# Kernel tuning notes

Hardware: AMD Instinct MI355X
Metric: run time of the kernel (lower is better)

The kernel has to match this reference:

```python
import jax, jax.numpy as jnp
import numpy as np

EPS = 1e-5
NUM_GROUPS = 8


def setup_inputs() -> dict:
    key = jax.random.key(0)
    ks = jax.random.split(key, 7)
    B, C, D, H, W = 2, 128, 16, 16, 16
    s = 1.0 / np.sqrt(C)
    return {
        "x": jax.random.normal(ks[0], (B, C, D, H, W), dtype=jnp.float32),
        "Wq": jax.random.normal(ks[1], (C, C), dtype=jnp.float32) * s,
        "Wk": jax.random.normal(ks[2], (C, C), dtype=jnp.float32) * s,
        "Wv": jax.random.normal(ks[3], (C, C), dtype=jnp.float32) * s,
        "Wo": jax.random.normal(ks[4], (C, C), dtype=jnp.float32) * s,
        "gamma": jnp.ones((C,), dtype=jnp.float32),
        "beta": jnp.zeros((C,), dtype=jnp.float32),
    }


def reference(x, Wq, Wk, Wv, Wo, gamma, beta):
    B, C = x.shape[0], x.shape[1]
    spatial = x.shape[2:]
    xf = x.reshape(B, C, -1)  # [B, C, N]

    # 1x1 conv == channel-mixing matmul
    q = jnp.einsum('oc,bcn->bon', Wq, xf)
    k = jnp.einsum('oc,bcn->bon', Wk, xf)
    v = jnp.einsum('oc,bcn->bon', Wv, xf)

    # unscaled attention: qk[b,n,m] = sum_c q[b,c,n] k[b,c,m]
    w = jax.nn.softmax(jnp.einsum('bcn,bcm->bnm', q, k), axis=-1)  # [B, N, N]
    # h = v @ w^T : h[b,c,n] = sum_m v[b,c,m] w[b,n,m]
    h = jnp.einsum('bcm,bnm->bcn', v, w)
    h = jnp.einsum('oc,bcn->bon', Wo, h)

    y = xf + h
    # GroupNorm(8, C) over (C//G, N) per group
    g = y.reshape(B, NUM_GROUPS, C // NUM_GROUPS, -1)
    mu = jnp.mean(g, axis=(2, 3), keepdims=True)
    var = jnp.mean(jnp.square(g - mu), axis=(2, 3), keepdims=True)
    gn = ((g - mu) * jax.lax.rsqrt(var + EPS)).reshape(B, C, -1)
    out = gn * gamma[None, :, None] + beta[None, :, None]
    out = out * jax.nn.sigmoid(out)  # SiLU
    return out.reshape(B, C, *spatial)
```

## Files before the change

kernel.cpp:

```cpp
#include <hip/hip_runtime.h>

#define CC 128
#define NN 4096
#define NB 2
#define TK 64
#define ITERS 32

typedef unsigned short ushort;
typedef unsigned int uint;
typedef __attribute__((ext_vector_type(8))) _Float16 h8;
typedef __attribute__((ext_vector_type(8))) short s8;
typedef __attribute__((ext_vector_type(4))) float f4;
#define MFMA16(a, b, c) __builtin_amdgcn_mfma_f32_16x16x32_f16(a, b, c, 0, 0, 0)
#define MFMAB(a, b, c)  __builtin_amdgcn_mfma_f32_16x16x32_bf16(a, b, c, 0, 0, 0)

__device__ __forceinline__ ushort f2h(float f) {
  _Float16 h = (_Float16)f;
  return *(ushort*)&h;
}
__device__ __forceinline__ ushort f2bf(float f) {
  uint u = __float_as_uint(f);
  u += 0x7fffu + ((u >> 16) & 1u);
  return (ushort)(u >> 16);
}

__global__ __launch_bounds__(256) void qkv_mm(
    const float* __restrict__ x, const float* __restrict__ Wq,
    const float* __restrict__ Wk, const float* __restrict__ Wv,
    ushort* __restrict__ qT, ushort* __restrict__ kT, ushort* __restrict__ vB,
    float* __restrict__ stats) {
  __shared__ ushort Wh[CC][136];
  __shared__ ushort xs[64][136];
  const int t = threadIdx.x;
  const int n0 = blockIdx.x * 64;
  const int which = blockIdx.y;
  const int b = blockIdx.z;
  const float* W = (which == 0) ? Wq : (which == 1) ? Wk : Wv;

  if (blockIdx.x == 0 && which == 0 && b == 0 && t < 32) stats[t] = 0.f;

#pragma unroll
  for (int i = 0; i < 16; ++i) {
    int slot = t + 256 * i;
    int o = slot >> 5, c4 = (slot & 31) * 4;
    float4 w4 = *(const float4*)&W[o * CC + c4];
    ushort4 p; p.x = f2h(w4.x); p.y = f2h(w4.y); p.z = f2h(w4.z); p.w = f2h(w4.w);
    *(ushort4*)&Wh[o][c4] = p;
  }
#pragma unroll
  for (int j = 0; j < 2; ++j) {
    int u = t + 256 * j;
    int c0 = (u & 31) * 4;
    int n4 = (u >> 5) * 4;
    float4 r0 = *(const float4*)&x[((size_t)b * CC + c0 + 0) * NN + n0 + n4];
    float4 r1 = *(const float4*)&x[((size_t)b * CC + c0 + 1) * NN + n0 + n4];
    float4 r2 = *(const float4*)&x[((size_t)b * CC + c0 + 2) * NN + n0 + n4];
    float4 r3 = *(const float4*)&x[((size_t)b * CC + c0 + 3) * NN + n0 + n4];
    ushort4 w0, w1, w2, w3;
    w0.x = f2h(r0.x); w0.y = f2h(r1.x); w0.z = f2h(r2.x); w0.w = f2h(r3.x);
    w1.x = f2h(r0.y); w1.y = f2h(r1.y); w1.z = f2h(r2.y); w1.w = f2h(r3.y);
    w2.x = f2h(r0.z); w2.y = f2h(r1.z); w2.z = f2h(r2.z); w2.w = f2h(r3.z);
    w3.x = f2h(r0.w); w3.y = f2h(r1.w); w3.z = f2h(r2.w); w3.w = f2h(r3.w);
    *(ushort4*)&xs[n4 + 0][c0] = w0;
    *(ushort4*)&xs[n4 + 1][c0] = w1;
    *(ushort4*)&xs[n4 + 2][c0] = w2;
    *(ushort4*)&xs[n4 + 3][c0] = w3;
  }
  __syncthreads();

  const int wv = t >> 6, lane = t & 63;
  const int quad = lane >> 4, l16 = lane & 15;

  if (which < 2) {
    ushort* out = (which == 0) ? qT : kT;
    f4 acc[2][4];
#pragma unroll
    for (int ot = 0; ot < 2; ++ot)
#pragma unroll
      for (int nt = 0; nt < 4; ++nt) acc[ot][nt] = (f4){0.f, 0.f, 0.f, 0.f};
#pragma unroll
    for (int kk = 0; kk < 4; ++kk) {
      h8 a0 = *(const h8*)&Wh[(wv * 2 + 0) * 16 + l16][kk * 32 + quad * 8];
      h8 a1 = *(const h8*)&Wh[(wv * 2 + 1) * 16 + l16][kk * 32 + quad * 8];
#pragma unroll
      for (int nt = 0; nt < 4; ++nt) {
        h8 bb = *(const h8*)&xs[nt * 16 + l16][kk * 32 + quad * 8];
        acc[0][nt] = MFMA16(a0, bb, acc[0][nt]);
        acc[1][nt] = MFMA16(a1, bb, acc[1][nt]);
      }
    }
#pragma unroll
    for (int ot = 0; ot < 2; ++ot)
#pragma unroll
      for (int nt = 0; nt < 4; ++nt) {
        f4 a = acc[ot][nt];
        ushort4 p; p.x = f2h(a[0]); p.y = f2h(a[1]); p.z = f2h(a[2]); p.w = f2h(a[3]);
        *(ushort4*)&out[((size_t)b * NN + n0 + nt * 16 + l16) * CC +
                        (wv * 2 + ot) * 16 + quad * 4] = p;
      }
  } else {
    f4 acc[8];
#pragma unroll
    for (int ct = 0; ct < 8; ++ct) acc[ct] = (f4){0.f, 0.f, 0.f, 0.f};
#pragma unroll
    for (int kk = 0; kk < 4; ++kk) {
      h8 a = *(const h8*)&xs[wv * 16 + l16][kk * 32 + quad * 8];
#pragma unroll
      for (int ct = 0; ct < 8; ++ct) {
        h8 bb = *(const h8*)&Wh[ct * 16 + l16][kk * 32 + quad * 8];
        acc[ct] = MFMA16(a, bb, acc[ct]);
      }
    }
#pragma unroll
    for (int ct = 0; ct < 8; ++ct) {
      f4 a = acc[ct];
      ushort4 p; p.x = f2bf(a[0]); p.y = f2bf(a[1]); p.z = f2bf(a[2]); p.w = f2bf(a[3]);
      *(ushort4*)&vB[((size_t)b * CC + ct * 16 + l16) * NN + n0 +
                     wv * 16 + quad * 4] = p;
    }
  }
}

__global__ __launch_bounds__(256) void attn_split(
    const ushort* __restrict__ qTg, const ushort* __restrict__ kTg,
    const ushort* __restrict__ vBg, float* __restrict__ O0,
    float* __restrict__ O1, float* __restrict__ Lg) {
  __shared__ ushort qsT[64][136];
  __shared__ ushort ksT[TK][136];
  __shared__ ushort vs[CC][72];
  __shared__ ushort psb[4][16][72];

  const int t = threadIdx.x;
  const int b = blockIdx.z;
  const int split = blockIdx.y;
  const int n0 = blockIdx.x * 64;
  const int wv = t >> 6;
  const int lane = t & 63;
  const int quad = lane >> 4;
  const int l16 = lane & 15;
  const int nw = n0 + wv * 16;
  float* Og = (split == 0) ? O0 : O1;

  {
    int qrow = t >> 2, qcol = (t & 3) * 32;
    size_t gq = ((size_t)b * NN + n0 + qrow) * CC + qcol;
    *(int4*)&qsT[qrow][qcol]      = *(const int4*)&qTg[gq];
    *(int4*)&qsT[qrow][qcol + 8]  = *(const int4*)&qTg[gq + 8];
    *(int4*)&qsT[qrow][qcol + 16] = *(const int4*)&qTg[gq + 16];
    *(int4*)&qsT[qrow][qcol + 24] = *(const int4*)&qTg[gq + 24];
  }

  const int krow = t >> 4, kcol = (t & 15) * 8;
  const int vrow = t >> 3, vcol = (t & 7) * 8;
  const ushort* kbp = kTg + ((size_t)b * NN + split * 2048 + krow) * CC + kcol;
  const ushort* vbp = vBg + ((size_t)b * CC + vrow) * NN + split * 2048 + vcol;

  int4 k0 = *(const int4*)&kbp[0];
  int4 k1 = *(const int4*)&kbp[16 * CC];
  int4 k2 = *(const int4*)&kbp[32 * CC];
  int4 k3 = *(const int4*)&kbp[48 * CC];
  int4 v0 = *(const int4*)&vbp[0];
  int4 v1 = *(const int4*)&vbp[(size_t)32 * NN];
  int4 v2 = *(const int4*)&vbp[(size_t)64 * NN];
  int4 v3 = *(const int4*)&vbp[(size_t)96 * NN];
  __syncthreads();

  h8 aq0 = *(const h8*)&qsT[wv * 16 + l16][0 * 32 + quad * 8];
  h8 aq1 = *(const h8*)&qsT[wv * 16 + l16][1 * 32 + quad * 8];
  h8 aq2 = *(const h8*)&qsT[wv * 16 + l16][2 * 32 + quad * 8];
  h8 aq3 = *(const h8*)&qsT[wv * 16 + l16][3 * 32 + quad * 8];

  s8 ones;
#pragma unroll
  for (int i = 0; i < 8; ++i) ones[i] = (short)0x3F80;

  f4 o0 = {0,0,0,0}, o1 = {0,0,0,0}, o2 = {0,0,0,0}, o3 = {0,0,0,0};
  f4 o4 = {0,0,0,0}, o5 = {0,0,0,0}, o6 = {0,0,0,0}, o7 = {0,0,0,0};
  f4 oL = {0,0,0,0};

  for (int kt = 0; kt < ITERS; ++kt) {
    *(int4*)&ksT[krow][kcol]      = k0;
    *(int4*)&ksT[krow + 16][kcol] = k1;
    *(int4*)&ksT[krow + 32][kcol] = k2;
    *(int4*)&ksT[krow + 48][kcol] = k3;
    *(int4*)&vs[vrow][vcol]       = v0;
    *(int4*)&vs[vrow + 32][vcol]  = v1;
    *(int4*)&vs[vrow + 64][vcol]  = v2;
    *(int4*)&vs[vrow + 96][vcol]  = v3;
    __syncthreads();

    {
      int ktn = (kt + 1 < ITERS) ? kt + 1 : kt;
      const ushort* kp = kbp + (size_t)ktn * TK * CC;
      const ushort* vp = vbp + (size_t)ktn * TK;
      k0 = *(const int4*)&kp[0];
      k1 = *(const int4*)&kp[16 * CC];
      k2 = *(const int4*)&kp[32 * CC];
      k3 = *(const int4*)&kp[48 * CC];
      v0 = *(const int4*)&vp[0];
      v1 = *(const int4*)&vp[(size_t)32 * NN];
      v2 = *(const int4*)&vp[(size_t)64 * NN];
      v3 = *(const int4*)&vp[(size_t)96 * NN];
    }

    f4 s0 = {0,0,0,0}, s1 = {0,0,0,0}, s2 = {0,0,0,0}, s3 = {0,0,0,0};
#pragma unroll
    for (int kk = 0; kk < 4; ++kk) {
      h8 a = (kk == 0) ? aq0 : (kk == 1) ? aq1 : (kk == 2) ? aq2 : aq3;
      h8 b0 = *(const h8*)&ksT[l16][kk * 32 + quad * 8];
      h8 b1 = *(const h8*)&ksT[16 + l16][kk * 32 + quad * 8];
      h8 b2 = *(const h8*)&ksT[32 + l16][kk * 32 + quad * 8];
      h8 b3 = *(const h8*)&ksT[48 + l16][kk * 32 + quad * 8];
      s0 = MFMA16(a, b0, s0);
      s1 = MFMA16(a, b1, s1);
      s2 = MFMA16(a, b2, s2);
      s3 = MFMA16(a, b3, s3);
    }

#pragma unroll
    for (int r = 0; r < 4; ++r) {
      int row = quad * 4 + r;
      psb[wv][row][l16]      = f2bf(__expf(s0[r]));
      psb[wv][row][16 + l16] = f2bf(__expf(s1[r]));
      psb[wv][row][32 + l16] = f2bf(__expf(s2[r]));
      psb[wv][row][48 + l16] = f2bf(__expf(s3[r]));
    }

#pragma unroll
    for (int mk = 0; mk < 2; ++mk) {
      s8 bp = *(const s8*)&psb[wv][l16][mk * 32 + quad * 8];
      s8 a0 = *(const s8*)&vs[0 * 16 + l16][mk * 32 + quad * 8];
      s8 a1 = *(const s8*)&vs[1 * 16 + l16][mk * 32 + quad * 8];
      s8 a2 = *(const s8*)&vs[2 * 16 + l16][mk * 32 + quad * 8];
      s8 a3 = *(const s8*)&vs[3 * 16 + l16][mk * 32 + quad * 8];
      o0 = MFMAB(a0, bp, o0);
      o1 = MFMAB(a1, bp, o1);
      o2 = MFMAB(a2, bp, o2);
      o3 = MFMAB(a3, bp, o3);
      s8 a4 = *(const s8*)&vs[4 * 16 + l16][mk * 32 + quad * 8];
      s8 a5 = *(const s8*)&vs[5 * 16 + l16][mk * 32 + quad * 8];
      s8 a6 = *(const s8*)&vs[6 * 16 + l16][mk * 32 + quad * 8];
      s8 a7 = *(const s8*)&vs[7 * 16 + l16][mk * 32 + quad * 8];
      o4 = MFMAB(a4, bp, o4);
      o5 = MFMAB(a5, bp, o5);
      o6 = MFMAB(a6, bp, o6);
      o7 = MFMAB(a7, bp, o7);
      oL = MFMAB(ones, bp, oL);
    }
    __syncthreads();
  }

  if (quad == 0)
    Lg[((size_t)(b * 2 + split)) * NN + nw + l16] = oL[0];
  {
    size_t nb_ = ((size_t)b * NN + nw + l16) * CC + quad * 4;
    *(f4*)&Og[nb_ + 0 * 16] = o0;
    *(f4*)&Og[nb_ + 1 * 16] = o1;
    *(f4*)&Og[nb_ + 2 * 16] = o2;
    *(f4*)&Og[nb_ + 3 * 16] = o3;
    *(f4*)&Og[nb_ + 4 * 16] = o4;
    *(f4*)&Og[nb_ + 5 * 16] = o5;
    *(f4*)&Og[nb_ + 6 * 16] = o6;
    *(f4*)&Og[nb_ + 7 * 16] = o7;
  }
}

__global__ __launch_bounds__(256) void proj_mm(
    const float* __restrict__ x, const float* __restrict__ Wo,
    const float* __restrict__ O0, const float* __restrict__ O1,
    const float* __restrict__ Lg, float* __restrict__ y,
    float* __restrict__ stats) {
  __shared__ ushort Wh[CC][136];
  __shared__ ushort hT[32][136];
  __shared__ float Linv[32];
  const int t = threadIdx.x;
  const int n0 = blockIdx.x * 32;
  const int b = blockIdx.y;

#pragma unroll
  for (int i = 0; i < 16; ++i) {
    int slot = t + 256 * i;
    int o = slot >> 5, c4 = (slot & 31) * 4;
    float4 w4 = *(const float4*)&Wo[o * CC + c4];
    ushort4 p; p.x = f2h(w4.x); p.y = f2h(w4.y); p.z = f2h(w4.z); p.w = f2h(w4.w);
    *(ushort4*)&Wh[o][c4] = p;
  }
  if (t < 32)
    Linv[t] = 1.f / (Lg[(size_t)(b * 2 + 0) * NN + n0 + t] +
                     Lg[(size_t)(b * 2 + 1) * NN + n0 + t]);
  __syncthreads();

#pragma unroll
  for (int i = 0; i < 16; ++i) {
    int slot = t + 256 * i;
    int n = slot >> 5, c4 = (slot & 31) * 4;
    size_t off = ((size_t)b * NN + n0 + n) * CC + c4;
    float4 a = *(const float4*)&O0[off];
    float4 bb = *(const float4*)&O1[off];
    float li = Linv[n];
    ushort4 p;
    p.x = f2h((a.x + bb.x) * li); p.y = f2h((a.y + bb.y) * li);
    p.z = f2h((a.z + bb.z) * li); p.w = f2h((a.w + bb.w) * li);
    *(ushort4*)&hT[n][c4] = p;
  }
  __syncthreads();

  const int wv = t >> 6, lane = t & 63;
  const int quad = lane >> 4, l16 = lane & 15;

  f4 acc[2][2];
#pragma unroll
  for (int nt = 0; nt < 2; ++nt)
#pragma unroll
    for (int ot = 0; ot < 2; ++ot) acc[nt][ot] = (f4){0.f, 0.f, 0.f, 0.f};
#pragma unroll
  for (int kk = 0; kk < 4; ++kk) {
    h8 a0 = *(const h8*)&hT[0 * 16 + l16][kk * 32 + quad * 8];
    h8 a1 = *(const h8*)&hT[1 * 16 + l16][kk * 32 + quad * 8];
    h8 b0 = *(const h8*)&Wh[(wv * 2 + 0) * 16 + l16][kk * 32 + quad * 8];
    h8 b1 = *(const h8*)&Wh[(wv * 2 + 1) * 16 + l16][kk * 32 + quad * 8];
    acc[0][0] = MFMA16(a0, b0, acc[0][0]);
    acc[0][1] = MFMA16(a0, b1, acc[0][1]);
    acc[1][0] = MFMA16(a1, b0, acc[1][0]);
    acc[1][1] = MFMA16(a1, b1, acc[1][1]);
  }

#pragma unroll
  for (int ot = 0; ot < 2; ++ot) {
    const int o = (wv * 2 + ot) * 16 + l16;
    const int g = wv * 2 + ot;
    float s = 0.f, sq = 0.f;
#pragma unroll
    for (int nt = 0; nt < 2; ++nt) {
      size_t addr = ((size_t)b * CC + o) * NN + n0 + nt * 16 + quad * 4;
      float4 xv = *(const float4*)&x[addr];
      f4 a = acc[nt][ot];
      float4 yy;
      yy.x = a[0] + xv.x; yy.y = a[1] + xv.y;
      yy.z = a[2] + xv.z; yy.w = a[3] + xv.w;
      *(float4*)&y[addr] = yy;
      s += yy.x + yy.y + yy.z + yy.w;
      sq += yy.x * yy.x + yy.y * yy.y + yy.z * yy.z + yy.w * yy.w;
    }
#pragma unroll
    for (int off = 1; off < 64; off <<= 1) {
      s += __shfl_xor(s, off);
      sq += __shfl_xor(sq, off);
    }
    if (lane == 0) {
      atomicAdd(&stats[(b * 8 + g) * 2 + 0], s);
      atomicAdd(&stats[(b * 8 + g) * 2 + 1], sq);
    }
  }
}

__global__ __launch_bounds__(256) void gn_silu(
    const float* __restrict__ y, const float* __restrict__ stats,
    const float* __restrict__ gamma, const float* __restrict__ beta,
    float* __restrict__ out) {
  const int tid = blockIdx.x * 256 + threadIdx.x;
  const int i4 = tid * 4;
  const int c = (i4 >> 12) & (CC - 1);
  const int b = i4 >> 19;
  const int g = c >> 4;
  const float inv = 1.f / 65536.f;
  float sum = stats[(b * 8 + g) * 2 + 0];
  float sq  = stats[(b * 8 + g) * 2 + 1];
  float mean = sum * inv;
  float var = sq * inv - mean * mean;
  float rs = rsqrtf(var + 1e-5f);
  float ga = gamma[c], be = beta[c];
  float4 v4 = *(const float4*)&y[i4];
  float4 r;
  float o;
  o = (v4.x - mean) * rs * ga + be; r.x = o / (1.f + __expf(-o));
  o = (v4.y - mean) * rs * ga + be; r.y = o / (1.f + __expf(-o));
  o = (v4.z - mean) * rs * ga + be; r.z = o / (1.f + __expf(-o));
  o = (v4.w - mean) * rs * ga + be; r.w = o / (1.f + __expf(-o));
  *(float4*)&out[i4] = r;
}

extern "C" void kernel_launch(void* const* d_in, const int* in_sizes, int n_in,
                              void* d_out, int out_size, void* d_ws, size_t ws_size,
                              hipStream_t stream) {
  const float* x     = (const float*)d_in[0];
  const float* Wq    = (const float*)d_in[1];
  const float* Wk    = (const float*)d_in[2];
  const float* Wv    = (const float*)d_in[3];
  const float* Wo    = (const float*)d_in[4];
  const float* gamma = (const float*)d_in[5];
  const float* beta  = (const float*)d_in[6];
  float* out = (float*)d_out;
  float* ws  = (float*)d_ws;

  const size_t M = (size_t)NB * CC * NN;
  float* Osp1 = ws;
  float* Osp0 = ws + M;
  ushort* qT = (ushort*)(ws + 2 * M);
  ushort* kT = qT + M;
  float* y = ws + 2 * M;
  ushort* vB = kT + M;
  float* Lg = (float*)(vB + M);
  float* stats = Lg + 2 * NN * NB;

  qkv_mm<<<dim3(NN / 64, 3, NB), 256, 0, stream>>>(x, Wq, Wk, Wv, qT, kT, vB, stats);
  attn_split<<<dim3(NN / 64, 2, NB), 256, 0, stream>>>(qT, kT, vB, Osp0, Osp1, Lg);
  proj_mm<<<dim3(NN / 32, NB), 256, 0, stream>>>(x, Wo, Osp0, Osp1, Lg, y, stats);
  gn_silu<<<dim3((int)(M / 1024)), 256, 0, stream>>>(y, stats, gamma, beta, out);
}
```

Measured before the change: 156.9 us.

## Split attention keys four ways with smaller tiles and bf16 partial outputs

The attention kernel now splits the key range into four chunks instead of two, which doubles the grid to 512 blocks, and halves the key tile to 32 keys. Partial outputs are stored as bf16 instead of fp32, and Q fragments are loaded straight from global memory instead of being staged through shared memory. proj_mm now sums four bf16 partials and four partial row sums. The goal is better occupancy and less LDS use, and the combine traffic stays about the same as before. In exchange, partial sums lose precision, and each iteration does half the MFMA work per barrier, so synchronisation overhead rises.

```diff
diff --git a/kernel.cpp b/kernel.cpp
--- a/kernel.cpp
+++ b/kernel.cpp
@@ -3,7 +3,8 @@
 #define CC 128
 #define NN 4096
 #define NB 2
-#define TK 64
+#define NSPLIT 4
+#define TK 32
 #define ITERS 32
 
 typedef unsigned short ushort;
@@ -22,6 +23,9 @@
   uint u = __float_as_uint(f);
   u += 0x7fffu + ((u >> 16) & 1u);
   return (ushort)(u >> 16);
+}
+__device__ __forceinline__ float bf2f(ushort u) {
+  return __uint_as_float((uint)u << 16);
 }
 
 __global__ __launch_bounds__(256) void qkv_mm(
@@ -123,12 +127,11 @@
 
 __global__ __launch_bounds__(256) void attn_split(
     const ushort* __restrict__ qTg, const ushort* __restrict__ kTg,
-    const ushort* __restrict__ vBg, float* __restrict__ O0,
-    float* __restrict__ O1, float* __restrict__ Lg) {
-  __shared__ ushort qsT[64][136];
+    const ushort* __restrict__ vBg, ushort* __restrict__ Op,
+    float* __restrict__ Lg) {
   __shared__ ushort ksT[TK][136];
-  __shared__ ushort vs[CC][72];
-  __shared__ ushort psb[4][16][72];
+  __shared__ ushort vs[CC][40];
+  __shared__ ushort psb[4][16][44];
 
   const int t = threadIdx.x;
   const int b = blockIdx.z;
@@ -139,36 +142,23 @@
   const int quad = lane >> 4;
   const int l16 = lane & 15;
   const int nw = n0 + wv * 16;
-  float* Og = (split == 0) ? O0 : O1;
-
-  {
-    int qrow = t >> 2, qcol = (t & 3) * 32;
-    size_t gq = ((size_t)b * NN + n0 + qrow) * CC + qcol;
-    *(int4*)&qsT[qrow][qcol]      = *(const int4*)&qTg[gq];
-    *(int4*)&qsT[qrow][qcol + 8]  = *(const int4*)&qTg[gq + 8];
-    *(int4*)&qsT[qrow][qcol + 16] = *(const int4*)&qTg[gq + 16];
-    *(int4*)&qsT[qrow][qcol + 24] = *(const int4*)&qTg[gq + 24];
-  }
-
-  const int krow = t >> 4, kcol = (t & 15) * 8;
-  const int vrow = t >> 3, vcol = (t & 7) * 8;
-  const ushort* kbp = kTg + ((size_t)b * NN + split * 2048 + krow) * CC + kcol;
-  const ushort* vbp = vBg + ((size_t)b * CC + vrow) * NN + split * 2048 + vcol;
+  const int m00 = split * (NN / NSPLIT);
+
+  const int krow = t >> 3, kcol = (t & 7) * 8;
+  const int vrow = t >> 1, vcol = (t & 1) * 16;
+  const ushort* kbp = kTg + ((size_t)b * NN + m00 + krow) * CC + kcol;
+  const ushort* vbp = vBg + ((size_t)b * CC + vrow) * NN + m00 + vcol;
+
+  const size_t qb = ((size_t)b * NN + nw + l16) * CC + quad * 8;
+  h8 aq0 = *(const h8*)&qTg[qb + 0 * 32];
+  h8 aq1 = *(const h8*)&qTg[qb + 1 * 32];
+  h8 aq2 = *(const h8*)&qTg[qb + 2 * 32];
+  h8 aq3 = *(const h8*)&qTg[qb + 3 * 32];
 
   int4 k0 = *(const int4*)&kbp[0];
-  int4 k1 = *(const int4*)&kbp[16 * CC];
-  int4 k2 = *(const int4*)&kbp[32 * CC];
-  int4 k3 = *(const int4*)&kbp[48 * CC];
+  int4 k1 = *(const int4*)&kbp[64];
   int4 v0 = *(const int4*)&vbp[0];
-  int4 v1 = *(const int4*)&vbp[(size_t)32 * NN];
-  int4 v2 = *(const int4*)&vbp[(size_t)64 * NN];
-  int4 v3 = *(const int4*)&vbp[(size_t)96 * NN];
-  __syncthreads();
-
-  h8 aq0 = *(const h8*)&qsT[wv * 16 + l16][0 * 32 + quad * 8];
-  h8 aq1 = *(const h8*)&qsT[wv * 16 + l16][1 * 32 + quad * 8];
-  h8 aq2 = *(const h8*)&qsT[wv * 16 + l16][2 * 32 + quad * 8];
-  h8 aq3 = *(const h8*)&qsT[wv * 16 + l16][3 * 32 + quad * 8];
+  int4 v1 = *(const int4*)&vbp[8];
 
   s8 ones;
 #pragma unroll
@@ -180,13 +170,9 @@
 
   for (int kt = 0; kt < ITERS; ++kt) {
     *(int4*)&ksT[krow][kcol]      = k0;
-    *(int4*)&ksT[krow + 16][kcol] = k1;
-    *(int4*)&ksT[krow + 32][kcol] = k2;
-    *(int4*)&ksT[krow + 48][kcol] = k3;
+    *(int4*)&ksT[krow][kcol + 64] = k1;
     *(int4*)&vs[vrow][vcol]       = v0;
-    *(int4*)&vs[vrow + 32][vcol]  = v1;
-    *(int4*)&vs[vrow + 64][vcol]  = v2;
-    *(int4*)&vs[vrow + 96][vcol]  = v3;
+    *(int4*)&vs[vrow][vcol + 8]   = v1;
     __syncthreads();
 
     {
@@ -194,27 +180,19 @@
       const ushort* kp = kbp + (size_t)ktn * TK * CC;
       const ushort* vp = vbp + (size_t)ktn * TK;
       k0 = *(const int4*)&kp[0];
-      k1 = *(const int4*)&kp[16 * CC];
-      k2 = *(const int4*)&kp[32 * CC];
-      k3 = *(const int4*)&kp[48 * CC];
+      k1 = *(const int4*)&kp[64];
       v0 = *(const int4*)&vp[0];
-      v1 = *(const int4*)&vp[(size_t)32 * NN];
-      v2 = *(const int4*)&vp[(size_t)64 * NN];
-      v3 = *(const int4*)&vp[(size_t)96 * NN];
-    }
-
-    f4 s0 = {0,0,0,0}, s1 = {0,0,0,0}, s2 = {0,0,0,0}, s3 = {0,0,0,0};
+      v1 = *(const int4*)&vp[8];
+    }
+
+    f4 s0 = {0,0,0,0}, s1 = {0,0,0,0};
 #pragma unroll
     for (int kk = 0; kk < 4; ++kk) {
       h8 a = (kk == 0) ? aq0 : (kk == 1) ? aq1 : (kk == 2) ? aq2 : aq3;
       h8 b0 = *(const h8*)&ksT[l16][kk * 32 + quad * 8];
       h8 b1 = *(const h8*)&ksT[16 + l16][kk * 32 + quad * 8];
-      h8 b2 = *(const h8*)&ksT[32 + l16][kk * 32 + quad * 8];
-      h8 b3 = *(const h8*)&ksT[48 + l16][kk * 32 + quad * 8];
       s0 = MFMA16(a, b0, s0);
       s1 = MFMA16(a, b1, s1);
-      s2 = MFMA16(a, b2, s2);
-      s3 = MFMA16(a, b3, s3);
     }
 
 #pragma unroll
@@ -222,25 +200,22 @@
       int row = quad * 4 + r;
       psb[wv][row][l16]      = f2bf(__expf(s0[r]));
       psb[wv][row][16 + l16] = f2bf(__expf(s1[r]));
-      psb[wv][row][32 + l16] = f2bf(__expf(s2[r]));
-      psb[wv][row][48 + l16] = f2bf(__expf(s3[r]));
-    }
-
-#pragma unroll
-    for (int mk = 0; mk < 2; ++mk) {
-      s8 bp = *(const s8*)&psb[wv][l16][mk * 32 + quad * 8];
-      s8 a0 = *(const s8*)&vs[0 * 16 + l16][mk * 32 + quad * 8];
-      s8 a1 = *(const s8*)&vs[1 * 16 + l16][mk * 32 + quad * 8];
-      s8 a2 = *(const s8*)&vs[2 * 16 + l16][mk * 32 + quad * 8];
-      s8 a3 = *(const s8*)&vs[3 * 16 + l16][mk * 32 + quad * 8];
+    }
+
+    {
+      s8 bp = *(const s8*)&psb[wv][l16][quad * 8];
+      s8 a0 = *(const s8*)&vs[0 * 16 + l16][quad * 8];
+      s8 a1 = *(const s8*)&vs[1 * 16 + l16][quad * 8];
+      s8 a2 = *(const s8*)&vs[2 * 16 + l16][quad * 8];
+      s8 a3 = *(const s8*)&vs[3 * 16 + l16][quad * 8];
       o0 = MFMAB(a0, bp, o0);
       o1 = MFMAB(a1, bp, o1);
       o2 = MFMAB(a2, bp, o2);
       o3 = MFMAB(a3, bp, o3);
-      s8 a4 = *(const s8*)&vs[4 * 16 + l16][mk * 32 + quad * 8];
-      s8 a5 = *(const s8*)&vs[5 * 16 + l16][mk * 32 + quad * 8];
-      s8 a6 = *(const s8*)&vs[6 * 16 + l16][mk * 32 + quad * 8];
-      s8 a7 = *(const s8*)&vs[7 * 16 + l16][mk * 32 + quad * 8];
+      s8 a4 = *(const s8*)&vs[4 * 16 + l16][quad * 8];
+      s8 a5 = *(const s8*)&vs[5 * 16 + l16][quad * 8];
+      s8 a6 = *(const s8*)&vs[6 * 16 + l16][quad * 8];
+      s8 a7 = *(const s8*)&vs[7 * 16 + l16][quad * 8];
       o4 = MFMAB(a4, bp, o4);
       o5 = MFMAB(a5, bp, o5);
       o6 = MFMAB(a6, bp, o6);
@@ -251,25 +226,23 @@
   }
 
   if (quad == 0)
-    Lg[((size_t)(b * 2 + split)) * NN + nw + l16] = oL[0];
+    Lg[((size_t)(split * NB + b)) * NN + nw + l16] = oL[0];
   {
-    size_t nb_ = ((size_t)b * NN + nw + l16) * CC + quad * 4;
-    *(f4*)&Og[nb_ + 0 * 16] = o0;
-    *(f4*)&Og[nb_ + 1 * 16] = o1;
-    *(f4*)&Og[nb_ + 2 * 16] = o2;
-    *(f4*)&Og[nb_ + 3 * 16] = o3;
-    *(f4*)&Og[nb_ + 4 * 16] = o4;
-    *(f4*)&Og[nb_ + 5 * 16] = o5;
-    *(f4*)&Og[nb_ + 6 * 16] = o6;
-    *(f4*)&Og[nb_ + 7 * 16] = o7;
+    size_t nb_ = ((size_t)(split * NB + b) * NN + nw + l16) * CC + quad * 4;
+    ushort4 p;
+#define STORE_O(oo, off) \
+    p.x = f2bf(oo[0]); p.y = f2bf(oo[1]); p.z = f2bf(oo[2]); p.w = f2bf(oo[3]); \
+    *(ushort4*)&Op[nb_ + off] = p;
+    STORE_O(o0, 0 * 16) STORE_O(o1, 1 * 16) STORE_O(o2, 2 * 16) STORE_O(o3, 3 * 16)
+    STORE_O(o4, 4 * 16) STORE_O(o5, 5 * 16) STORE_O(o6, 6 * 16) STORE_O(o7, 7 * 16)
+#undef STORE_O
   }
 }
 
 __global__ __launch_bounds__(256) void proj_mm(
     const float* __restrict__ x, const float* __restrict__ Wo,
-    const float* __restrict__ O0, const float* __restrict__ O1,
-    const float* __restrict__ Lg, float* __restrict__ y,
-    float* __restrict__ stats) {
+    const ushort* __restrict__ Op, const float* __restrict__ Lg,
+    float* __restrict__ y, float* __restrict__ stats) {
   __shared__ ushort Wh[CC][136];
   __shared__ ushort hT[32][136];
   __shared__ float Linv[32];
@@ -285,22 +258,30 @@
     ushort4 p; p.x = f2h(w4.x); p.y = f2h(w4.y); p.z = f2h(w4.z); p.w = f2h(w4.w);
     *(ushort4*)&Wh[o][c4] = p;
   }
-  if (t < 32)
-    Linv[t] = 1.f / (Lg[(size_t)(b * 2 + 0) * NN + n0 + t] +
-                     Lg[(size_t)(b * 2 + 1) * NN + n0 + t]);
+  if (t < 32) {
+    float l = 0.f;
+#pragma unroll
+    for (int s = 0; s < NSPLIT; ++s)
+      l += Lg[(size_t)(s * NB + b) * NN + n0 + t];
+    Linv[t] = 1.f / l;
+  }
   __syncthreads();
 
 #pragma unroll
   for (int i = 0; i < 16; ++i) {
     int slot = t + 256 * i;
     int n = slot >> 5, c4 = (slot & 31) * 4;
-    size_t off = ((size_t)b * NN + n0 + n) * CC + c4;
-    float4 a = *(const float4*)&O0[off];
-    float4 bb = *(const float4*)&O1[off];
+    size_t base = ((size_t)(n0 + n)) * CC + c4;
+    float a0 = 0.f, a1 = 0.f, a2 = 0.f, a3 = 0.f;
+#pragma unroll
+    for (int s = 0; s < NSPLIT; ++s) {
+      ushort4 u = *(const ushort4*)&Op[(size_t)(s * NB + b) * NN * CC + base];
+      a0 += bf2f(u.x); a1 += bf2f(u.y); a2 += bf2f(u.z); a3 += bf2f(u.w);
+    }
     float li = Linv[n];
     ushort4 p;
-    p.x = f2h((a.x + bb.x) * li); p.y = f2h((a.y + bb.y) * li);
-    p.z = f2h((a.z + bb.z) * li); p.w = f2h((a.w + bb.w) * li);
+    p.x = f2h(a0 * li); p.y = f2h(a1 * li);
+    p.z = f2h(a2 * li); p.w = f2h(a3 * li);
     *(ushort4*)&hT[n][c4] = p;
   }
   __syncthreads();
@@ -394,17 +375,16 @@
   float* ws  = (float*)d_ws;
 
   const size_t M = (size_t)NB * CC * NN;
-  float* Osp1 = ws;
-  float* Osp0 = ws + M;
+  ushort* Op = (ushort*)ws;
   ushort* qT = (ushort*)(ws + 2 * M);
   ushort* kT = qT + M;
   float* y = ws + 2 * M;
   ushort* vB = kT + M;
   float* Lg = (float*)(vB + M);
-  float* stats = Lg + 2 * NN * NB;
+  float* stats = Lg + (size_t)NSPLIT * NB * NN;
 
   qkv_mm<<<dim3(NN / 64, 3, NB), 256, 0, stream>>>(x, Wq, Wk, Wv, qT, kT, vB, stats);
-  attn_split<<<dim3(NN / 64, 2, NB), 256, 0, stream>>>(qT, kT, vB, Osp0, Osp1, Lg);
-  proj_mm<<<dim3(NN / 32, NB), 256, 0, stream>>>(x, Wo, Osp0, Osp1, Lg, y, stats);
+  attn_split<<<dim3(NN / 64, NSPLIT, NB), 256, 0, stream>>>(qT, kT, vB, Op, Lg);
+  proj_mm<<<dim3(NN / 32, NB), 256, 0, stream>>>(x, Wo, Op, Lg, y, stats);
   gn_silu<<<dim3((int)(M / 1024)), 256, 0, stream>>>(y, stats, gamma, beta, out);
 }
```

New measurement: 149.5 us. 1.05x faster.
